# Performance work log

Measured on AMD Instinct MI355X. Metric: run time of the kernel, lower is better.

## Reference

```python
import jax, jax.numpy as jnp
import numpy as np

# E2M1 (FP4) value table: low 3 bits magnitude, bit 3 sign (indices 8..15 negative)
FP4_TABLE = jnp.array([0.0, 0.5, 1.0, 1.5, 2.0, 3.0, 4.0, 6.0,
                       0.0, -0.5, -1.0, -1.5, -2.0, -3.0, -4.0, -6.0], dtype=jnp.float32)
FP4_BLOCK = 32  # per-row 1x32 scale groups


def dequant_fp4(packed, scale):
    """packed: [E, O, I//2] uint8 (two e2m1 nibbles per byte, low nibble first),
    scale: [E, O, I//32] float32 (e8m0, i.e. powers of two). Returns [E, O, I] float32."""
    lo = (packed & 15).astype(jnp.int32)
    hi = ((packed >> 4) & 15).astype(jnp.int32)
    # interleave low, high nibbles along the input dim (matches torch stack(...,-1).flatten)
    vals = FP4_TABLE[jnp.stack([lo, hi], axis=-1)]  # [E, O, I//2, 2]
    w = vals.reshape(packed.shape[0], packed.shape[1], packed.shape[2] * 2)
    return w * jnp.repeat(scale, FP4_BLOCK, axis=-1)


def setup_inputs() -> dict:
    T, H, F, E, K = 2048, 2048, 1024, 16, 4
    key = jax.random.key(0)
    k = jax.random.split(key, 8)
    hidden_states = jax.random.normal(k[0], (T, H), dtype=jnp.float32)
    topk_weights = jax.nn.softmax(jax.random.normal(k[1], (T, K)), axis=-1)
    topk_ids = jax.random.randint(k[2], (T, K), 0, E, dtype=jnp.int32)
    # checkpoint-native packed FP4 expert weights + e8m0 (power-of-two) scales
    gate_up_weight = jax.random.randint(k[3], (E, 2 * F, H // 2), 0, 256, dtype=jnp.int32).astype(jnp.uint8)
    gate_up_scale = jnp.exp2(jax.random.randint(k[4], (E, 2 * F, H // 32), -8, -5).astype(jnp.float32))
    down_weight = jax.random.randint(k[5], (E, H, F // 2), 0, 256, dtype=jnp.int32).astype(jnp.uint8)
    down_scale = jnp.exp2(jax.random.randint(k[6], (E, H, F // 32), -8, -5).astype(jnp.float32))
    return {"hidden_states": hidden_states, "topk_weights": topk_weights, "topk_ids": topk_ids,
            "gate_up_weight": gate_up_weight, "gate_up_scale": gate_up_scale,
            "down_weight": down_weight, "down_scale": down_scale}


def reference(hidden_states, topk_weights, topk_ids, gate_up_weight, gate_up_scale, down_weight, down_scale):
    # 1. dequantize checkpoint-native FP4 experts to dense float weights
    w_gate_up = dequant_fp4(gate_up_weight, gate_up_scale)  # [E, 2F, H]
    w_down = dequant_fp4(down_weight, down_scale)           # [E, H, F]
    T = hidden_states.shape[0]
    E = w_gate_up.shape[0]
    # 2. scatter routing weights into a dense [T, E] combine matrix
    combine = jnp.zeros((T, E), dtype=hidden_states.dtype)
    combine = combine.at[jnp.arange(T)[:, None], topk_ids].add(topk_weights)
    # 3. grouped expert GEMM (exact dense dispatch over experts)
    gu = jnp.einsum('th,eoh->teo', hidden_states, w_gate_up)  # [T, E, 2F]
    gate, up = jnp.split(gu, 2, axis=-1)                       # gate = first ffn_dim rows
    act = jax.nn.silu(gate) * up                               # SwiGLU (swiglu_limit=0 -> no clamping)
    act = act * combine[:, :, None]                            # fold routing weights into activations
    return jnp.einsum('tef,ehf->th', act, w_down)              # [T, H]
```

## Files before the change

### kernel.cpp

```cpp
#include <hip/hip_runtime.h>
#include <stdint.h>

#define HD 2048
#define FD 1024
#define NE 16
#define NPAIR 8192
#define BM 256
#define MAXT 48
#define LDK 40

typedef short bf16x8 __attribute__((ext_vector_type(8)));
typedef float f32x4 __attribute__((ext_vector_type(4)));
typedef unsigned short u16;

static __device__ __forceinline__ u16 f2bf(float f) {
  uint32_t u = __float_as_uint(f);
  u += 0x7FFFu + ((u >> 16) & 1u);
  return (u16)(u >> 16);
}

struct DqTab { uint32_t hA, hB, lA, lB; };

static __device__ __forceinline__ DqTab make_tab(uint32_t sbits) {
  int n = (int)(sbits >> 23) - 127;
  int q = n >> 1;
  uint32_t r = (uint32_t)(n & 1);
  uint32_t mq = (uint32_t)(-q);
  uint32_t sub1 = mq * 0x01010100u;
  uint32_t subA = mq * 0x01010101u;
  DqTab t;
  t.hA = (r ? 0x40403F00u : 0x3F3F3F00u) - sub1;
  t.hB = (r ? 0x41414040u : 0x40404040u) - subA;
  t.lA = r ? 0x40008000u : 0xC0800000u;
  t.lB = r ? 0x4000C080u : 0xC0804000u;
  return t;
}

static __device__ __forceinline__ void dq8(uint32_t p, const DqTab& t, uint32_t* d) {
  uint32_t a = p & 0x0F0F0F0Fu;
  uint32_t b = (p >> 4) & 0x0F0F0F0Fu;
  uint32_t x0 = __builtin_amdgcn_perm(b, a, 0x05010400u);
  uint32_t x1 = __builtin_amdgcn_perm(b, a, 0x07030602u);
  uint32_t m0 = x0 & 0x07070707u;
  uint32_t m1 = x1 & 0x07070707u;
  uint32_t h0 = __builtin_amdgcn_perm(t.hB, t.hA, m0) | ((x0 & 0x08080808u) << 4);
  uint32_t h1 = __builtin_amdgcn_perm(t.hB, t.hA, m1) | ((x1 & 0x08080808u) << 4);
  uint32_t l0 = __builtin_amdgcn_perm(t.lB, t.lA, m0);
  uint32_t l1 = __builtin_amdgcn_perm(t.lB, t.lA, m1);
  d[0] = __builtin_amdgcn_perm(h0, l0, 0x05010400u);
  d[1] = __builtin_amdgcn_perm(h0, l0, 0x07030602u);
  d[2] = __builtin_amdgcn_perm(h1, l1, 0x05010400u);
  d[3] = __builtin_amdgcn_perm(h1, l1, 0x07030602u);
}

static __device__ __forceinline__ uint32_t pack4(int4 v) {
  return (uint32_t)(v.x & 0xFF) | ((uint32_t)(v.y & 0xFF) << 8) |
         ((uint32_t)(v.z & 0xFF) << 16) | ((uint32_t)v.w << 24);
}

__global__ void cast_kernel(const float* __restrict__ x, u16* __restrict__ xb) {
  int i = blockIdx.x * 256 + threadIdx.x;
  float4 v = ((const float4*)x)[i];
  ushort4 o;
  o.x = f2bf(v.x); o.y = f2bf(v.y); o.z = f2bf(v.z); o.w = f2bf(v.w);
  ((ushort4*)xb)[i] = o;
}

__global__ void zero_kernel(float4* __restrict__ out) {
  out[blockIdx.x * 256 + threadIdx.x] = float4{0.f, 0.f, 0.f, 0.f};
}

__global__ void route_kernel(const int* __restrict__ ids, const float* __restrict__ tw,
                             int* __restrict__ rows, float* __restrict__ rw,
                             int* __restrict__ te) {
  __shared__ int cnt[NE], base[NE], run[NE];
  int tid = threadIdx.x;
  if (tid < NE) { cnt[tid] = 0; run[tid] = 0; }
  __syncthreads();
  for (int i = tid; i < NPAIR; i += 256) atomicAdd(&cnt[ids[i]], 1);
  __syncthreads();
  if (tid == 0) {
    int cum = 0;
    for (int e = 0; e < NE; ++e) {
      base[e] = cum;
      int nt = (cnt[e] + BM - 1) >> 8;
      for (int j = 0; j < nt; ++j) te[(cum >> 8) + j] = e;
      cum += nt << 8;
    }
    for (int t = cum >> 8; t < MAXT; ++t) te[t] = -1;
  }
  __syncthreads();
  for (int i = tid; i < MAXT * BM; i += 256) { rows[i] = -1; rw[i] = 0.f; }
  __syncthreads();
  for (int i = tid; i < NPAIR; i += 256) {
    int e = ids[i];
    int p = base[e] + atomicAdd(&run[e], 1);
    rows[p] = i >> 2;
    rw[p] = tw[i];
  }
}

__global__ __launch_bounds__(256, 2) void gemm1_kernel(
    const u16* __restrict__ xb, const int* __restrict__ gup32,
    const uint32_t* __restrict__ gus, const int* __restrict__ rows,
    const float* __restrict__ rw, const int* __restrict__ te,
    u16* __restrict__ act) {
  const int tile = blockIdx.y;
  const int e = te[tile];
  if (e < 0) return;
  const int f0 = blockIdx.x * 64;

  __shared__ u16 sA[2][BM * LDK];
  __shared__ u16 sBg[2][64 * LDK];
  __shared__ u16 sBu[2][64 * LDK];
  __shared__ int rows_s[BM];
  __shared__ float rw_s[BM];

  const int tid = threadIdx.x;
  rows_s[tid] = rows[tile * BM + tid];
  rw_s[tid] = rw[tile * BM + tid];
  __syncthreads();

  int arow = rows_s[tid];
  arow = arow < 0 ? 0 : arow;
  const u16* aptr = xb + (size_t)arow * HD;
  const int lofsA = tid * LDK;

  const int bn = (tid & 127) >> 1;
  const int isUp = tid >> 7;
  const int o = isUp * 1024 + f0 + bn;
  const int skh = tid & 1;
  const int* bptr = gup32 + (size_t)(e * 2048 + o) * (HD / 2) + skh * 8;
  const uint32_t* sptr = gus + (size_t)(e * 2048 + o) * (HD / 32);
  const int lofsB = bn * LDK + skh * 16;

  const int lane = tid & 63;
  const int w = tid >> 6;
  const int q = lane >> 4, c = lane & 15;

  f32x4 Cg[4][4], Cu[4][4];
#pragma unroll
  for (int s = 0; s < 4; ++s)
#pragma unroll
    for (int t2 = 0; t2 < 4; ++t2) {
      Cg[s][t2] = f32x4{0.f, 0.f, 0.f, 0.f};
      Cu[s][t2] = f32x4{0.f, 0.f, 0.f, 0.f};
    }

  {
    uint4 a0 = *(const uint4*)(aptr);
    uint4 a1 = *(const uint4*)(aptr + 8);
    uint4 a2 = *(const uint4*)(aptr + 16);
    uint4 a3 = *(const uint4*)(aptr + 24);
    int4 w0 = *(const int4*)(bptr);
    int4 w1 = *(const int4*)(bptr + 4);
    uint32_t sb = sptr[0];
    DqTab t = make_tab(sb);
    uint32_t d0[4], d1[4];
    dq8(pack4(w0), t, d0);
    dq8(pack4(w1), t, d1);
    u16* sAp = &sA[0][lofsA];
    *(uint4*)sAp = a0;
    *(uint4*)(sAp + 8) = a1;
    *(uint4*)(sAp + 16) = a2;
    *(uint4*)(sAp + 24) = a3;
    u16* sBp = (isUp ? sBu[0] : sBg[0]) + lofsB;
    *(uint4*)sBp = make_uint4(d0[0], d0[1], d0[2], d0[3]);
    *(uint4*)(sBp + 8) = make_uint4(d1[0], d1[1], d1[2], d1[3]);
  }

  for (int kk = 0; kk < HD / 32; ++kk) {
    const int p = kk & 1;
    __syncthreads();
    uint4 na0, na1, na2, na3;
    int4 nw0, nw1;
    uint32_t nsb;
    if (kk < HD / 32 - 1) {
      const int k2 = (kk + 1) * 32;
      na0 = *(const uint4*)(aptr + k2);
      na1 = *(const uint4*)(aptr + k2 + 8);
      na2 = *(const uint4*)(aptr + k2 + 16);
      na3 = *(const uint4*)(aptr + k2 + 24);
      nw0 = *(const int4*)(bptr + (k2 >> 1));
      nw1 = *(const int4*)(bptr + (k2 >> 1) + 4);
      nsb = sptr[k2 >> 5];
    }

    bf16x8 af[4], bg[4], bu[4];
#pragma unroll
    for (int s = 0; s < 4; ++s)
      af[s] = *(const bf16x8*)&sA[p][(w * 64 + s * 16 + c) * LDK + q * 8];
#pragma unroll
    for (int t2 = 0; t2 < 4; ++t2) {
      bg[t2] = *(const bf16x8*)&sBg[p][(t2 * 16 + c) * LDK + q * 8];
      bu[t2] = *(const bf16x8*)&sBu[p][(t2 * 16 + c) * LDK + q * 8];
    }
#pragma unroll
    for (int s = 0; s < 4; ++s)
#pragma unroll
      for (int t2 = 0; t2 < 4; ++t2) {
        Cg[s][t2] = __builtin_amdgcn_mfma_f32_16x16x32_bf16(af[s], bg[t2], Cg[s][t2], 0, 0, 0);
        Cu[s][t2] = __builtin_amdgcn_mfma_f32_16x16x32_bf16(af[s], bu[t2], Cu[s][t2], 0, 0, 0);
      }

    if (kk < HD / 32 - 1) {
      DqTab t = make_tab(nsb);
      uint32_t d0[4], d1[4];
      dq8(pack4(nw0), t, d0);
      dq8(pack4(nw1), t, d1);
      u16* sAp = &sA[p ^ 1][lofsA];
      *(uint4*)sAp = na0;
      *(uint4*)(sAp + 8) = na1;
      *(uint4*)(sAp + 16) = na2;
      *(uint4*)(sAp + 24) = na3;
      u16* sBp = (isUp ? sBu[p ^ 1] : sBg[p ^ 1]) + lofsB;
      *(uint4*)sBp = make_uint4(d0[0], d0[1], d0[2], d0[3]);
      *(uint4*)(sBp + 8) = make_uint4(d1[0], d1[1], d1[2], d1[3]);
    }
  }

#pragma unroll
  for (int s = 0; s < 4; ++s) {
    const int mlb = w * 64 + s * 16 + q * 4;
#pragma unroll
    for (int t2 = 0; t2 < 4; ++t2) {
      const int fg = f0 + t2 * 16 + c;
#pragma unroll
      for (int r = 0; r < 4; ++r) {
        const int ml = mlb + r;
        float g = Cg[s][t2][r];
        float u = Cu[s][t2][r];
        float aval = g / (1.f + __expf(-g)) * u * rw_s[ml];
        act[(size_t)(tile * BM + ml) * FD + fg] = f2bf(aval);
      }
    }
  }
}

__global__ __launch_bounds__(256, 2) void gemm2_kernel(
    const u16* __restrict__ act, const int* __restrict__ dwn32,
    const uint32_t* __restrict__ dsc, const int* __restrict__ rows,
    const int* __restrict__ te, float* __restrict__ out) {
  const int tile = blockIdx.y;
  const int e = te[tile];
  if (e < 0) return;
  const int h0 = blockIdx.x * 128;

  __shared__ u16 sA[2][BM * LDK];
  __shared__ u16 sB[2][128 * LDK];
  __shared__ int rows_s[BM];

  const int tid = threadIdx.x;
  rows_s[tid] = rows[tile * BM + tid];
  __syncthreads();

  const u16* aptr = act + (size_t)(tile * BM + tid) * FD;
  const int lofsA = tid * LDK;

  const int bn = tid >> 1;
  const int skh = tid & 1;
  const int* bptr = dwn32 + (size_t)(e * 2048 + h0 + bn) * (FD / 2) + skh * 8;
  const uint32_t* sptr = dsc + (size_t)(e * 2048 + h0 + bn) * (FD / 32);
  const int lofsB = bn * LDK + skh * 16;

  const int lane = tid & 63;
  const int w = tid >> 6;
  const int q = lane >> 4, c = lane & 15;

  f32x4 Cd[4][8];
#pragma unroll
  for (int s = 0; s < 4; ++s)
#pragma unroll
    for (int t2 = 0; t2 < 8; ++t2) Cd[s][t2] = f32x4{0.f, 0.f, 0.f, 0.f};

  {
    uint4 a0 = *(const uint4*)(aptr);
    uint4 a1 = *(const uint4*)(aptr + 8);
    uint4 a2 = *(const uint4*)(aptr + 16);
    uint4 a3 = *(const uint4*)(aptr + 24);
    int4 w0 = *(const int4*)(bptr);
    int4 w1 = *(const int4*)(bptr + 4);
    uint32_t sb = sptr[0];
    DqTab t = make_tab(sb);
    uint32_t d0[4], d1[4];
    dq8(pack4(w0), t, d0);
    dq8(pack4(w1), t, d1);
    u16* sAp = &sA[0][lofsA];
    *(uint4*)sAp = a0;
    *(uint4*)(sAp + 8) = a1;
    *(uint4*)(sAp + 16) = a2;
    *(uint4*)(sAp + 24) = a3;
    u16* sBp = sB[0] + lofsB;
    *(uint4*)sBp = make_uint4(d0[0], d0[1], d0[2], d0[3]);
    *(uint4*)(sBp + 8) = make_uint4(d1[0], d1[1], d1[2], d1[3]);
  }

  for (int kk = 0; kk < FD / 32; ++kk) {
    const int p = kk & 1;
    __syncthreads();
    uint4 na0, na1, na2, na3;
    int4 nw0, nw1;
    uint32_t nsb;
    if (kk < FD / 32 - 1) {
      const int k2 = (kk + 1) * 32;
      na0 = *(const uint4*)(aptr + k2);
      na1 = *(const uint4*)(aptr + k2 + 8);
      na2 = *(const uint4*)(aptr + k2 + 16);
      na3 = *(const uint4*)(aptr + k2 + 24);
      nw0 = *(const int4*)(bptr + (k2 >> 1));
      nw1 = *(const int4*)(bptr + (k2 >> 1) + 4);
      nsb = sptr[k2 >> 5];
    }

    bf16x8 af[4], bf_[8];
#pragma unroll
    for (int s = 0; s < 4; ++s)
      af[s] = *(const bf16x8*)&sA[p][(w * 64 + s * 16 + c) * LDK + q * 8];
#pragma unroll
    for (int t2 = 0; t2 < 8; ++t2)
      bf_[t2] = *(const bf16x8*)&sB[p][(t2 * 16 + c) * LDK + q * 8];
#pragma unroll
    for (int s = 0; s < 4; ++s)
#pragma unroll
      for (int t2 = 0; t2 < 8; ++t2)
        Cd[s][t2] = __builtin_amdgcn_mfma_f32_16x16x32_bf16(af[s], bf_[t2], Cd[s][t2], 0, 0, 0);

    if (kk < FD / 32 - 1) {
      DqTab t = make_tab(nsb);
      uint32_t d0[4], d1[4];
      dq8(pack4(nw0), t, d0);
      dq8(pack4(nw1), t, d1);
      u16* sAp = &sA[p ^ 1][lofsA];
      *(uint4*)sAp = na0;
      *(uint4*)(sAp + 8) = na1;
      *(uint4*)(sAp + 16) = na2;
      *(uint4*)(sAp + 24) = na3;
      u16* sBp = sB[p ^ 1] + lofsB;
      *(uint4*)sBp = make_uint4(d0[0], d0[1], d0[2], d0[3]);
      *(uint4*)(sBp + 8) = make_uint4(d1[0], d1[1], d1[2], d1[3]);
    }
  }

#pragma unroll
  for (int s = 0; s < 4; ++s) {
    const int mlb = w * 64 + s * 16 + q * 4;
#pragma unroll
    for (int t2 = 0; t2 < 8; ++t2) {
      const int hg = h0 + t2 * 16 + c;
#pragma unroll
      for (int r = 0; r < 4; ++r) {
        int token = rows_s[mlb + r];
        if (token >= 0) atomicAdd(&out[(size_t)token * HD + hg], Cd[s][t2][r]);
      }
    }
  }
}

extern "C" void kernel_launch(void* const* d_in, const int* in_sizes, int n_in,
                              void* d_out, int out_size, void* d_ws, size_t ws_size,
                              hipStream_t stream) {
  const float* hidden = (const float*)d_in[0];
  const float* tw = (const float*)d_in[1];
  const int* ids = (const int*)d_in[2];
  const int* gup32 = (const int*)d_in[3];
  const uint32_t* gus = (const uint32_t*)d_in[4];
  const int* dwn32 = (const int*)d_in[5];
  const uint32_t* dsc = (const uint32_t*)d_in[6];
  float* out = (float*)d_out;

  char* ws = (char*)d_ws;
  int* rows = (int*)(ws);
  float* rw = (float*)(ws + 49152);
  int* te = (int*)(ws + 98304);
  u16* xb = (u16*)(ws + 131072);
  u16* act = (u16*)(ws + 8519680);

  cast_kernel<<<dim3(4096), dim3(256), 0, stream>>>(hidden, xb);
  zero_kernel<<<dim3(4096), dim3(256), 0, stream>>>((float4*)out);
  route_kernel<<<dim3(1), dim3(256), 0, stream>>>(ids, tw, rows, rw, te);
  gemm1_kernel<<<dim3(16, MAXT), dim3(256), 0, stream>>>(xb, gup32, gus, rows, rw, te, act);
  gemm2_kernel<<<dim3(16, MAXT), dim3(256), 0, stream>>>(act, dwn32, dsc, rows, te, out);
}
```

Measured before the change: 583.5 us.

## Shrink M tiles, widen N tiles, load A fragments directly from global

```diff
diff --git a/kernel.cpp b/kernel.cpp
--- a/kernel.cpp
+++ b/kernel.cpp
@@ -5,8 +5,8 @@
 #define FD 1024
 #define NE 16
 #define NPAIR 8192
-#define BM 256
-#define MAXT 48
+#define BM 128
+#define MAXT 80
 #define LDK 40
 
 typedef short bf16x8 __attribute__((ext_vector_type(8)));
@@ -83,11 +83,11 @@
     int cum = 0;
     for (int e = 0; e < NE; ++e) {
       base[e] = cum;
-      int nt = (cnt[e] + BM - 1) >> 8;
-      for (int j = 0; j < nt; ++j) te[(cum >> 8) + j] = e;
-      cum += nt << 8;
-    }
-    for (int t = cum >> 8; t < MAXT; ++t) te[t] = -1;
+      int nt = (cnt[e] + BM - 1) >> 7;
+      for (int j = 0; j < nt; ++j) te[(cum >> 7) + j] = e;
+      cum += nt << 7;
+    }
+    for (int t = cum >> 7; t < MAXT; ++t) te[t] = -1;
   }
   __syncthreads();
   for (int i = tid; i < MAXT * BM; i += 256) { rows[i] = -1; rw[i] = 0.f; }
@@ -100,7 +100,7 @@
   }
 }
 
-__global__ __launch_bounds__(256, 2) void gemm1_kernel(
+__global__ __launch_bounds__(512, 4) void gemm1_kernel(
     const u16* __restrict__ xb, const int* __restrict__ gup32,
     const uint32_t* __restrict__ gus, const int* __restrict__ rows,
     const float* __restrict__ rw, const int* __restrict__ te,
@@ -108,50 +108,50 @@
   const int tile = blockIdx.y;
   const int e = te[tile];
   if (e < 0) return;
-  const int f0 = blockIdx.x * 64;
-
-  __shared__ u16 sA[2][BM * LDK];
-  __shared__ u16 sBg[2][64 * LDK];
-  __shared__ u16 sBu[2][64 * LDK];
+  const int f0 = blockIdx.x * 128;
+
+  __shared__ u16 sB[2][256 * LDK];
   __shared__ int rows_s[BM];
   __shared__ float rw_s[BM];
 
   const int tid = threadIdx.x;
-  rows_s[tid] = rows[tile * BM + tid];
-  rw_s[tid] = rw[tile * BM + tid];
-  __syncthreads();
-
-  int arow = rows_s[tid];
-  arow = arow < 0 ? 0 : arow;
-  const u16* aptr = xb + (size_t)arow * HD;
-  const int lofsA = tid * LDK;
-
-  const int bn = (tid & 127) >> 1;
-  const int isUp = tid >> 7;
-  const int o = isUp * 1024 + f0 + bn;
+  if (tid < BM) {
+    rows_s[tid] = rows[tile * BM + tid];
+    rw_s[tid] = rw[tile * BM + tid];
+  }
+  __syncthreads();
+
+  const int bn = tid >> 1;
   const int skh = tid & 1;
+  const int o = (bn < 128) ? (f0 + bn) : (1024 + f0 + (bn - 128));
   const int* bptr = gup32 + (size_t)(e * 2048 + o) * (HD / 2) + skh * 8;
   const uint32_t* sptr = gus + (size_t)(e * 2048 + o) * (HD / 32);
   const int lofsB = bn * LDK + skh * 16;
 
   const int lane = tid & 63;
   const int w = tid >> 6;
+  const int wr = w >> 2;
+  const int wc = w & 3;
   const int q = lane >> 4, c = lane & 15;
 
-  f32x4 Cg[4][4], Cu[4][4];
+  uint32_t aofs[4];
+#pragma unroll
+  for (int s = 0; s < 4; ++s) {
+    int r_ = rows_s[wr * 64 + s * 16 + c];
+    r_ = r_ < 0 ? 0 : r_;
+    aofs[s] = (uint32_t)r_ * HD + q * 8;
+  }
+
+  f32x4 Cg[4][2], Cu[4][2];
 #pragma unroll
   for (int s = 0; s < 4; ++s)
 #pragma unroll
-    for (int t2 = 0; t2 < 4; ++t2) {
+    for (int t2 = 0; t2 < 2; ++t2) {
       Cg[s][t2] = f32x4{0.f, 0.f, 0.f, 0.f};
       Cu[s][t2] = f32x4{0.f, 0.f, 0.f, 0.f};
     }
 
   {
-    uint4 a0 = *(const uint4*)(aptr);
-    uint4 a1 = *(const uint4*)(aptr + 8);
-    uint4 a2 = *(const uint4*)(aptr + 16);
-    uint4 a3 = *(const uint4*)(aptr + 24);
     int4 w0 = *(const int4*)(bptr);
     int4 w1 = *(const int4*)(bptr + 4);
     uint32_t sb = sptr[0];
@@ -159,12 +159,7 @@
     uint32_t d0[4], d1[4];
     dq8(pack4(w0), t, d0);
     dq8(pack4(w1), t, d1);
-    u16* sAp = &sA[0][lofsA];
-    *(uint4*)sAp = a0;
-    *(uint4*)(sAp + 8) = a1;
-    *(uint4*)(sAp + 16) = a2;
-    *(uint4*)(sAp + 24) = a3;
-    u16* sBp = (isUp ? sBu[0] : sBg[0]) + lofsB;
+    u16* sBp = sB[0] + lofsB;
     *(uint4*)sBp = make_uint4(d0[0], d0[1], d0[2], d0[3]);
     *(uint4*)(sBp + 8) = make_uint4(d1[0], d1[1], d1[2], d1[3]);
   }
@@ -172,48 +167,37 @@
   for (int kk = 0; kk < HD / 32; ++kk) {
     const int p = kk & 1;
     __syncthreads();
-    uint4 na0, na1, na2, na3;
     int4 nw0, nw1;
     uint32_t nsb;
     if (kk < HD / 32 - 1) {
-      const int k2 = (kk + 1) * 32;
-      na0 = *(const uint4*)(aptr + k2);
-      na1 = *(const uint4*)(aptr + k2 + 8);
-      na2 = *(const uint4*)(aptr + k2 + 16);
-      na3 = *(const uint4*)(aptr + k2 + 24);
-      nw0 = *(const int4*)(bptr + (k2 >> 1));
-      nw1 = *(const int4*)(bptr + (k2 >> 1) + 4);
-      nsb = sptr[k2 >> 5];
-    }
-
-    bf16x8 af[4], bg[4], bu[4];
+      const int kb = (kk + 1) * 16;
+      nw0 = *(const int4*)(bptr + kb);
+      nw1 = *(const int4*)(bptr + kb + 4);
+      nsb = sptr[kk + 1];
+    }
+
+    bf16x8 af[4];
 #pragma unroll
     for (int s = 0; s < 4; ++s)
-      af[s] = *(const bf16x8*)&sA[p][(w * 64 + s * 16 + c) * LDK + q * 8];
-#pragma unroll
-    for (int t2 = 0; t2 < 4; ++t2) {
-      bg[t2] = *(const bf16x8*)&sBg[p][(t2 * 16 + c) * LDK + q * 8];
-      bu[t2] = *(const bf16x8*)&sBu[p][(t2 * 16 + c) * LDK + q * 8];
-    }
-#pragma unroll
-    for (int s = 0; s < 4; ++s)
-#pragma unroll
-      for (int t2 = 0; t2 < 4; ++t2) {
-        Cg[s][t2] = __builtin_amdgcn_mfma_f32_16x16x32_bf16(af[s], bg[t2], Cg[s][t2], 0, 0, 0);
-        Cu[s][t2] = __builtin_amdgcn_mfma_f32_16x16x32_bf16(af[s], bu[t2], Cu[s][t2], 0, 0, 0);
+      af[s] = *(const bf16x8*)(xb + aofs[s] + kk * 32);
+
+#pragma unroll
+    for (int t2 = 0; t2 < 2; ++t2) {
+      bf16x8 bg = *(const bf16x8*)&sB[p][(wc * 32 + t2 * 16 + c) * LDK + q * 8];
+      bf16x8 bu = *(const bf16x8*)&sB[p][(128 + wc * 32 + t2 * 16 + c) * LDK + q * 8];
+#pragma unroll
+      for (int s = 0; s < 4; ++s) {
+        Cg[s][t2] = __builtin_amdgcn_mfma_f32_16x16x32_bf16(af[s], bg, Cg[s][t2], 0, 0, 0);
+        Cu[s][t2] = __builtin_amdgcn_mfma_f32_16x16x32_bf16(af[s], bu, Cu[s][t2], 0, 0, 0);
       }
+    }
 
     if (kk < HD / 32 - 1) {
       DqTab t = make_tab(nsb);
       uint32_t d0[4], d1[4];
       dq8(pack4(nw0), t, d0);
       dq8(pack4(nw1), t, d1);
-      u16* sAp = &sA[p ^ 1][lofsA];
-      *(uint4*)sAp = na0;
-      *(uint4*)(sAp + 8) = na1;
-      *(uint4*)(sAp + 16) = na2;
-      *(uint4*)(sAp + 24) = na3;
-      u16* sBp = (isUp ? sBu[p ^ 1] : sBg[p ^ 1]) + lofsB;
+      u16* sBp = sB[p ^ 1] + lofsB;
       *(uint4*)sBp = make_uint4(d0[0], d0[1], d0[2], d0[3]);
       *(uint4*)(sBp + 8) = make_uint4(d1[0], d1[1], d1[2], d1[3]);
     }
@@ -221,10 +205,10 @@
 
 #pragma unroll
   for (int s = 0; s < 4; ++s) {
-    const int mlb = w * 64 + s * 16 + q * 4;
-#pragma unroll
-    for (int t2 = 0; t2 < 4; ++t2) {
-      const int fg = f0 + t2 * 16 + c;
+    const int mlb = wr * 64 + s * 16 + q * 4;
+#pragma unroll
+    for (int t2 = 0; t2 < 2; ++t2) {
+      const int fg = f0 + wc * 32 + t2 * 16 + c;
 #pragma unroll
       for (int r = 0; r < 4; ++r) {
         const int ml = mlb + r;
@@ -237,47 +221,47 @@
   }
 }
 
-__global__ __launch_bounds__(256, 2) void gemm2_kernel(
+__global__ __launch_bounds__(512, 4) void gemm2_kernel(
     const u16* __restrict__ act, const int* __restrict__ dwn32,
     const uint32_t* __restrict__ dsc, const int* __restrict__ rows,
     const int* __restrict__ te, float* __restrict__ out) {
   const int tile = blockIdx.y;
   const int e = te[tile];
   if (e < 0) return;
-  const int h0 = blockIdx.x * 128;
-
-  __shared__ u16 sA[2][BM * LDK];
-  __shared__ u16 sB[2][128 * LDK];
+  const int h0 = blockIdx.x * 256;
+
+  __shared__ u16 sB[2][256 * LDK];
   __shared__ int rows_s[BM];
 
   const int tid = threadIdx.x;
-  rows_s[tid] = rows[tile * BM + tid];
-  __syncthreads();
-
-  const u16* aptr = act + (size_t)(tile * BM + tid) * FD;
-  const int lofsA = tid * LDK;
+  if (tid < BM) rows_s[tid] = rows[tile * BM + tid];
+  __syncthreads();
 
   const int bn = tid >> 1;
   const int skh = tid & 1;
-  const int* bptr = dwn32 + (size_t)(e * 2048 + h0 + bn) * (FD / 2) + skh * 8;
-  const uint32_t* sptr = dsc + (size_t)(e * 2048 + h0 + bn) * (FD / 32);
+  const int o = h0 + bn;
+  const int* bptr = dwn32 + (size_t)(e * 2048 + o) * (FD / 2) + skh * 8;
+  const uint32_t* sptr = dsc + (size_t)(e * 2048 + o) * (FD / 32);
   const int lofsB = bn * LDK + skh * 16;
 
   const int lane = tid & 63;
   const int w = tid >> 6;
+  const int wr = w >> 2;
+  const int wc = w & 3;
   const int q = lane >> 4, c = lane & 15;
 
-  f32x4 Cd[4][8];
+  uint32_t aofs[4];
 #pragma unroll
   for (int s = 0; s < 4; ++s)
-#pragma unroll
-    for (int t2 = 0; t2 < 8; ++t2) Cd[s][t2] = f32x4{0.f, 0.f, 0.f, 0.f};
+    aofs[s] = (uint32_t)(tile * BM + wr * 64 + s * 16 + c) * FD + q * 8;
+
+  f32x4 Cd[4][4];
+#pragma unroll
+  for (int s = 0; s < 4; ++s)
+#pragma unroll
+    for (int t2 = 0; t2 < 4; ++t2) Cd[s][t2] = f32x4{0.f, 0.f, 0.f, 0.f};
 
   {
-    uint4 a0 = *(const uint4*)(aptr);
-    uint4 a1 = *(const uint4*)(aptr + 8);
-    uint4 a2 = *(const uint4*)(aptr + 16);
-    uint4 a3 = *(const uint4*)(aptr + 24);
     int4 w0 = *(const int4*)(bptr);
     int4 w1 = *(const int4*)(bptr + 4);
     uint32_t sb = sptr[0];
@@ -285,11 +269,6 @@
     uint32_t d0[4], d1[4];
     dq8(pack4(w0), t, d0);
     dq8(pack4(w1), t, d1);
-    u16* sAp = &sA[0][lofsA];
-    *(uint4*)sAp = a0;
-    *(uint4*)(sAp + 8) = a1;
-    *(uint4*)(sAp + 16) = a2;
-    *(uint4*)(sAp + 24) = a3;
     u16* sBp = sB[0] + lofsB;
     *(uint4*)sBp = make_uint4(d0[0], d0[1], d0[2], d0[3]);
     *(uint4*)(sBp + 8) = make_uint4(d1[0], d1[1], d1[2], d1[3]);
@@ -298,43 +277,33 @@
   for (int kk = 0; kk < FD / 32; ++kk) {
     const int p = kk & 1;
     __syncthreads();
-    uint4 na0, na1, na2, na3;
     int4 nw0, nw1;
     uint32_t nsb;
     if (kk < FD / 32 - 1) {
-      const int k2 = (kk + 1) * 32;
-      na0 = *(const uint4*)(aptr + k2);
-      na1 = *(const uint4*)(aptr + k2 + 8);
-      na2 = *(const uint4*)(aptr + k2 + 16);
-      na3 = *(const uint4*)(aptr + k2 + 24);
-      nw0 = *(const int4*)(bptr + (k2 >> 1));
-      nw1 = *(const int4*)(bptr + (k2 >> 1) + 4);
-      nsb = sptr[k2 >> 5];
-    }
-
-    bf16x8 af[4], bf_[8];
+      const int kb = (kk + 1) * 16;
+      nw0 = *(const int4*)(bptr + kb);
+      nw1 = *(const int4*)(bptr + kb + 4);
+      nsb = sptr[kk + 1];
+    }
+
+    bf16x8 af[4];
 #pragma unroll
     for (int s = 0; s < 4; ++s)
-      af[s] = *(const bf16x8*)&sA[p][(w * 64 + s * 16 + c) * LDK + q * 8];
-#pragma unroll
-    for (int t2 = 0; t2 < 8; ++t2)
-      bf_[t2] = *(const bf16x8*)&sB[p][(t2 * 16 + c) * LDK + q * 8];
-#pragma unroll
-    for (int s = 0; s < 4; ++s)
-#pragma unroll
-      for (int t2 = 0; t2 < 8; ++t2)
-        Cd[s][t2] = __builtin_amdgcn_mfma_f32_16x16x32_bf16(af[s], bf_[t2], Cd[s][t2], 0, 0, 0);
+      af[s] = *(const bf16x8*)(act + aofs[s] + kk * 32);
+
+#pragma unroll
+    for (int t2 = 0; t2 < 4; ++t2) {
+      bf16x8 bf_ = *(const bf16x8*)&sB[p][(wc * 64 + t2 * 16 + c) * LDK + q * 8];
+#pragma unroll
+      for (int s = 0; s < 4; ++s)
+        Cd[s][t2] = __builtin_amdgcn_mfma_f32_16x16x32_bf16(af[s], bf_, Cd[s][t2], 0, 0, 0);
+    }
 
     if (kk < FD / 32 - 1) {
       DqTab t = make_tab(nsb);
       uint32_t d0[4], d1[4];
       dq8(pack4(nw0), t, d0);
       dq8(pack4(nw1), t, d1);
-      u16* sAp = &sA[p ^ 1][lofsA];
-      *(uint4*)sAp = na0;
-      *(uint4*)(sAp + 8) = na1;
-      *(uint4*)(sAp + 16) = na2;
-      *(uint4*)(sAp + 24) = na3;
       u16* sBp = sB[p ^ 1] + lofsB;
       *(uint4*)sBp = make_uint4(d0[0], d0[1], d0[2], d0[3]);
       *(uint4*)(sBp + 8) = make_uint4(d1[0], d1[1], d1[2], d1[3]);
@@ -343,10 +312,10 @@
 
 #pragma unroll
   for (int s = 0; s < 4; ++s) {
-    const int mlb = w * 64 + s * 16 + q * 4;
-#pragma unroll
-    for (int t2 = 0; t2 < 8; ++t2) {
-      const int hg = h0 + t2 * 16 + c;
+    const int mlb = wr * 64 + s * 16 + q * 4;
+#pragma unroll
+    for (int t2 = 0; t2 < 4; ++t2) {
+      const int hg = h0 + wc * 64 + t2 * 16 + c;
 #pragma unroll
       for (int r = 0; r < 4; ++r) {
         int token = rows_s[mlb + r];
@@ -378,6 +347,6 @@
   cast_kernel<<<dim3(4096), dim3(256), 0, stream>>>(hidden, xb);
   zero_kernel<<<dim3(4096), dim3(256), 0, stream>>>((float4*)out);
   route_kernel<<<dim3(1), dim3(256), 0, stream>>>(ids, tw, rows, rw, te);
-  gemm1_kernel<<<dim3(16, MAXT), dim3(256), 0, stream>>>(xb, gup32, gus, rows, rw, te, act);
-  gemm2_kernel<<<dim3(16, MAXT), dim3(256), 0, stream>>>(act, dwn32, dsc, rows, te, out);
-}
+  gemm1_kernel<<<dim3(8, MAXT), dim3(512), 0, stream>>>(xb, gup32, gus, rows, rw, te, act);
+  gemm2_kernel<<<dim3(8, MAXT), dim3(512), 0, stream>>>(act, dwn32, dsc, rows, te, out);
+}
```

Result: slower. 741.7 us (+27.1%).

## Replace gemm2 atomic scatter with per-pair stores and a reduction kernel

Applied to the files above, without the earlier changes.

```diff
diff --git a/kernel.cpp b/kernel.cpp
--- a/kernel.cpp
+++ b/kernel.cpp
@@ -72,7 +72,7 @@
 
 __global__ void route_kernel(const int* __restrict__ ids, const float* __restrict__ tw,
                              int* __restrict__ rows, float* __restrict__ rw,
-                             int* __restrict__ te) {
+                             int* __restrict__ te, int* __restrict__ pidx) {
   __shared__ int cnt[NE], base[NE], run[NE];
   int tid = threadIdx.x;
   if (tid < NE) { cnt[tid] = 0; run[tid] = 0; }
@@ -90,13 +90,18 @@
     for (int t = cum >> 8; t < MAXT; ++t) te[t] = -1;
   }
   __syncthreads();
-  for (int i = tid; i < MAXT * BM; i += 256) { rows[i] = -1; rw[i] = 0.f; }
+  for (int i = tid; i < MAXT * BM; i += 256) {
+    rows[i] = -1;
+    rw[i] = 0.f;
+    if (pidx) pidx[i] = -1;
+  }
   __syncthreads();
   for (int i = tid; i < NPAIR; i += 256) {
     int e = ids[i];
     int p = base[e] + atomicAdd(&run[e], 1);
     rows[p] = i >> 2;
     rw[p] = tw[i];
+    if (pidx) pidx[p] = i;
   }
 }
 
@@ -240,7 +245,8 @@
 __global__ __launch_bounds__(256, 2) void gemm2_kernel(
     const u16* __restrict__ act, const int* __restrict__ dwn32,
     const uint32_t* __restrict__ dsc, const int* __restrict__ rows,
-    const int* __restrict__ te, float* __restrict__ out) {
+    const int* __restrict__ pidx, const int* __restrict__ te,
+    float* __restrict__ out, float* __restrict__ pout) {
   const int tile = blockIdx.y;
   const int e = te[tile];
   if (e < 0) return;
@@ -249,9 +255,11 @@
   __shared__ u16 sA[2][BM * LDK];
   __shared__ u16 sB[2][128 * LDK];
   __shared__ int rows_s[BM];
+  __shared__ int pidx_s[BM];
 
   const int tid = threadIdx.x;
   rows_s[tid] = rows[tile * BM + tid];
+  pidx_s[tid] = pout ? pidx[tile * BM + tid] : -1;
   __syncthreads();
 
   const u16* aptr = act + (size_t)(tile * BM + tid) * FD;
@@ -341,19 +349,45 @@
     }
   }
 
-#pragma unroll
-  for (int s = 0; s < 4; ++s) {
-    const int mlb = w * 64 + s * 16 + q * 4;
-#pragma unroll
-    for (int t2 = 0; t2 < 8; ++t2) {
-      const int hg = h0 + t2 * 16 + c;
-#pragma unroll
-      for (int r = 0; r < 4; ++r) {
-        int token = rows_s[mlb + r];
-        if (token >= 0) atomicAdd(&out[(size_t)token * HD + hg], Cd[s][t2][r]);
+  if (pout) {
+#pragma unroll
+    for (int s = 0; s < 4; ++s) {
+      const int mlb = w * 64 + s * 16 + q * 4;
+#pragma unroll
+      for (int t2 = 0; t2 < 8; ++t2) {
+        const int hg = h0 + t2 * 16 + c;
+#pragma unroll
+        for (int r = 0; r < 4; ++r) {
+          int prow = pidx_s[mlb + r];
+          if (prow >= 0) pout[(size_t)prow * HD + hg] = Cd[s][t2][r];
+        }
       }
     }
-  }
+  } else {
+#pragma unroll
+    for (int s = 0; s < 4; ++s) {
+      const int mlb = w * 64 + s * 16 + q * 4;
+#pragma unroll
+      for (int t2 = 0; t2 < 8; ++t2) {
+        const int hg = h0 + t2 * 16 + c;
+#pragma unroll
+        for (int r = 0; r < 4; ++r) {
+          int token = rows_s[mlb + r];
+          if (token >= 0) atomicAdd(&out[(size_t)token * HD + hg], Cd[s][t2][r]);
+        }
+      }
+    }
+  }
+}
+
+__global__ void finalize_kernel(const float4* __restrict__ pout, float4* __restrict__ out) {
+  int j = blockIdx.x * 256 + threadIdx.x;
+  int token = j >> 9;
+  int col = j & 511;
+  const float4* p = pout + ((size_t)token * 4) * 512 + col;
+  float4 a = p[0], b = p[512], c = p[1024], d = p[1536];
+  out[j] = float4{a.x + b.x + c.x + d.x, a.y + b.y + c.y + d.y,
+                  a.z + b.z + c.z + d.z, a.w + b.w + c.w + d.w};
 }
 
 extern "C" void kernel_launch(void* const* d_in, const int* in_sizes, int n_in,
@@ -375,9 +409,17 @@
   u16* xb = (u16*)(ws + 131072);
   u16* act = (u16*)(ws + 8519680);
 
+  const size_t POUT_OFF = 33685504ULL;
+  const size_t PIDX_OFF = POUT_OFF + (size_t)NPAIR * HD * 4;
+  const size_t WS_NEED = PIDX_OFF + (size_t)MAXT * BM * 4;
+  const bool big = ws_size >= WS_NEED;
+  float* pout = big ? (float*)(ws + POUT_OFF) : nullptr;
+  int* pidx = big ? (int*)(ws + PIDX_OFF) : nullptr;
+
   cast_kernel<<<dim3(4096), dim3(256), 0, stream>>>(hidden, xb);
-  zero_kernel<<<dim3(4096), dim3(256), 0, stream>>>((float4*)out);
-  route_kernel<<<dim3(1), dim3(256), 0, stream>>>(ids, tw, rows, rw, te);
+  if (!big) zero_kernel<<<dim3(4096), dim3(256), 0, stream>>>((float4*)out);
+  route_kernel<<<dim3(1), dim3(256), 0, stream>>>(ids, tw, rows, rw, te, pidx);
   gemm1_kernel<<<dim3(16, MAXT), dim3(256), 0, stream>>>(xb, gup32, gus, rows, rw, te, act);
-  gemm2_kernel<<<dim3(16, MAXT), dim3(256), 0, stream>>>(act, dwn32, dsc, rows, te, out);
-}
+  gemm2_kernel<<<dim3(16, MAXT), dim3(256), 0, stream>>>(act, dwn32, dsc, rows, pidx, te, out, pout);
+  if (big) finalize_kernel<<<dim3(1024 * 1024 / 256), dim3(256), 0, stream>>>((const float4*)pout, (float4*)out);
+}
```

Measured after the change: 577.0 us. About the same (-1.1%).
